# Performance work log

Measured on AMD Instinct MI355X. Metric: run time of the kernel, lower is better.

Reference implementation:

```python
import jax, jax.numpy as jnp
import numpy as np

LAYERS, BLOCKS = 10, 4
RC, DC, SC, EC, CLASSES = 32, 32, 256, 256, 256
KS = 2
OUTPUT_LENGTH = 4096


def _dilations():
    ds = []
    init = 1
    for _b in range(BLOCKS):
        nd = 1
        for _i in range(LAYERS):
            ds.append((nd, init))
            init = nd
            nd *= 2
    return ds

DILATIONS = _dilations()


def dilate(x, dilation, init_dilation):
    # Faithful port of pytorch-wavenet dilate(): folds time into batch (or back)
    # by the ratio dilation/init_dilation, front-padding with zeros if needed.
    n, c, l = x.shape
    if dilation == init_dilation:
        return x
    if dilation > init_dilation:
        r = dilation // init_dilation
        new_l = -(-l // r) * r  # ceil to multiple of r
        if new_l != l:
            x = jnp.pad(x, ((0, 0), (0, 0), (new_l - l, 0)))  # pad_start=True
            l = new_l
        l_new, n_new = l // r, n * r
    else:
        r = init_dilation // dilation
        l_new, n_new = l * r, n // r
    x = jnp.transpose(x, (1, 2, 0)).reshape(c, l_new, n_new)  # (c, l, n) view
    return jnp.transpose(x, (2, 0, 1))


def conv2tap(x, w):
    # valid Conv1d, kernel_size=2, no bias; x: [n,c,l], w: [o,c,2]
    return jax.lax.conv_general_dilated(x, w, (1,), 'VALID',
                                        dimension_numbers=('NCH', 'OIH', 'NCH'))


def conv1x1(x, w):
    # 1x1 Conv1d as einsum; x: [n,c,l], w: [o,c]
    return jnp.einsum('ncl,oc->nol', x, w)


def setup_inputs() -> dict:
    key = jax.random.key(0)
    ks = jax.random.split(key, 10)
    nl = LAYERS * BLOCKS
    s = 0.05
    return {
        'x_input': jax.random.normal(ks[0], (8, CLASSES, 16384), jnp.float32),
        'start_w': jax.random.normal(ks[1], (RC, CLASSES, 1), jnp.float32) * s,
        'filter_w': jax.random.normal(ks[2], (nl, DC, RC, KS), jnp.float32) * s,
        'gate_w': jax.random.normal(ks[3], (nl, DC, RC, KS), jnp.float32) * s,
        'residual_w': jax.random.normal(ks[4], (nl, RC, DC, 1), jnp.float32) * s,
        'skip_w': jax.random.normal(ks[5], (nl, SC, DC, 1), jnp.float32) * s,
        'end1_w': jax.random.normal(ks[6], (EC, SC, 1), jnp.float32) * s,
        'end1_b': jnp.zeros((EC,), jnp.float32),
        'end2_w': jax.random.normal(ks[7], (CLASSES, EC, 1), jnp.float32) * s,
        'end2_b': jnp.zeros((CLASSES,), jnp.float32),
    }


def reference(x_input, start_w, filter_w, gate_w, residual_w, skip_w,
              end1_w, end1_b, end2_w, end2_b):
    x = conv1x1(x_input, start_w[:, :, 0])
    x_skip = None
    for i, (d, d0) in enumerate(DILATIONS):
        xr = dilate(x, d, d0)
        f = jnp.tanh(conv2tap(xr, filter_w[i]))
        g = jax.nn.sigmoid(conv2tap(xr, gate_w[i]))
        x = f * g
        xs = dilate(x, 1, d) if x.shape[2] != 1 else x
        # NOTE: the source never reassigns `skip`, so its try/except always
        # falls to the except branch and only the LAST layer's skip survives.
        x_skip = conv1x1(xs, skip_w[i][:, :, 0])
        x = conv1x1(x, residual_w[i][:, :, 0]) + xr[:, :, KS - 1:]
    y = jax.nn.relu(x_skip)
    y = jax.nn.relu(conv1x1(y, end1_w[:, :, 0]) + end1_b[None, :, None])
    y = conv1x1(y, end2_w[:, :, 0]) + end2_b[None, :, None]
    n, c, _l = y.shape
    y = y[:, :, -OUTPUT_LENGTH:]
    return jnp.transpose(y, (0, 2, 1)).reshape(n * OUTPUT_LENGTH, c)
```

## Files before the change

### kernel.cpp

```cpp
#include <hip/hip_runtime.h>
#include <hip/hip_bf16.h>
#include <math.h>


#define TS   8192
#define T0   8188
#define NB   8
#define RCH  32
#define CLS  256
#define TOUT 4096

#define OFF_WBLOB 0
#define OFF_ST    204800
#define OFF_SK    212992
#define OFF_E1T   221184
#define OFF_E2T   286720
#define OFF_XA    352256
#define OFF_XB    (OFF_XA + NB*RCH*TS)
#define OFF_H1    (OFF_XB + NB*RCH*TS)
#define OFF_E1    (OFF_H1 + NB*256*TOUT)

__device__ __forceinline__ float tanh_fast(float x) {
    float e = __expf(2.0f * x);
    return 1.0f - 2.0f / (e + 1.0f);
}
__device__ __forceinline__ float sigmoid_fast(float x) {
    return 1.0f / (1.0f + __expf(-x));
}

__global__ void repack_kernel(const float* __restrict__ start_w,
                              const float* __restrict__ filter_w,
                              const float* __restrict__ gate_w,
                              const float* __restrict__ residual_w,
                              const float* __restrict__ skip_w,
                              const float* __restrict__ end1_w,
                              const float* __restrict__ end2_w,
                              float* __restrict__ ws) {
    int id = blockIdx.x * 256 + threadIdx.x;
    if (id < 204800) {
        int l = id / 5120, r = id % 5120;
        float v;
        if (r < 4096) {
            const float* src = (r < 2048) ? filter_w : gate_w;
            int rr = r & 2047;
            int ic = rr >> 6, k = (rr >> 5) & 1, oc = rr & 31;
            v = src[((l * 32 + oc) * 32 + ic) * 2 + k];
        } else {
            int rr = r - 4096;
            int ic = rr >> 5, oc = rr & 31;
            v = residual_w[(l * 32 + oc) * 32 + ic];
        }
        ws[OFF_WBLOB + id] = v;
    } else if (id < 204800 + 8192) {
        int r = id - 204800;
        int ic = r >> 5, oc = r & 31;
        ws[OFF_ST + r] = start_w[oc * 256 + ic];
    } else if (id < 212992 + 8192) {
        int r = id - 212992;
        int dc = r >> 8, sc = r & 255;
        ws[OFF_SK + r] = skip_w[(39 * 256 + sc) * 32 + dc];
    } else if (id < 221184 + 65536) {
        int r = id - 221184;
        int sc = r >> 8, ec = r & 255;
        ws[OFF_E1T + r] = end1_w[ec * 256 + sc];
    } else if (id < 286720 + 65536) {
        int r = id - 286720;
        int ec = r >> 8, cc = r & 255;
        ws[OFF_E2T + r] = end2_w[cc * 256 + ec];
    }
}

__global__ __launch_bounds__(256) void start_kernel(const float* __restrict__ xin,
                                                    const float* __restrict__ st,
                                                    float* __restrict__ xout) {
    int t = blockIdx.x * 256 + threadIdx.x;
    int og = blockIdx.y;
    int b = blockIdx.z;
    if (t >= T0) return;
    const float* xi = xin + (size_t)b * 256 * 16384 + (16384 - T0) + t;
    const float* wb = st + og * 16;
    float acc[16];
#pragma unroll
    for (int c = 0; c < 16; c++) acc[c] = 0.f;
#pragma unroll 4
    for (int ic = 0; ic < 256; ic++) {
        float xv = xi[ic * 16384];
        const float* w = wb + ic * 32;
#pragma unroll
        for (int c = 0; c < 16; c++) acc[c] = fmaf(w[c], xv, acc[c]);
    }
    float* xo = xout + ((size_t)(b * RCH) + og * 16) * TS + t;
#pragma unroll
    for (int c = 0; c < 16; c++) xo[c * TS] = acc[c];
}

__global__ __launch_bounds__(256) void layer_kernel(const float* __restrict__ xin,
                                                    float* __restrict__ xout,
                                                    const float* __restrict__ wl,
                                                    int d, int Tout) {
    __shared__ float hs[32][64];
    int tx = threadIdx.x;
    int cg = __builtin_amdgcn_readfirstlane(threadIdx.y);
    int t  = blockIdx.x * 64 + tx;
    int b  = blockIdx.y;
    bool act = (t < Tout);

    const float* xi = xin + (size_t)(b * RCH) * TS + t;
    const float* wf = wl +        cg * 8;
    const float* wg = wl + 2048 + cg * 8;
    const float* wr = wl + 4096 + cg * 8;

    float accf[8], accg[8];
#pragma unroll
    for (int j = 0; j < 8; j++) { accf[j] = 0.f; accg[j] = 0.f; }

#pragma unroll 4
    for (int ic = 0; ic < 32; ic++) {
        float a = xi[ic * TS];
        float c = xi[ic * TS + d];
        const float* w0 = wf + ic * 64;
        const float* w1 = wg + ic * 64;
#pragma unroll
        for (int j = 0; j < 8; j++) accf[j] = fmaf(w0[j],      a, accf[j]);
#pragma unroll
        for (int j = 0; j < 8; j++) accf[j] = fmaf(w0[32 + j], c, accf[j]);
#pragma unroll
        for (int j = 0; j < 8; j++) accg[j] = fmaf(w1[j],      a, accg[j]);
#pragma unroll
        for (int j = 0; j < 8; j++) accg[j] = fmaf(w1[32 + j], c, accg[j]);
    }

#pragma unroll
    for (int j = 0; j < 8; j++)
        hs[cg * 8 + j][tx] = tanh_fast(accf[j]) * sigmoid_fast(accg[j]);
    __syncthreads();

    float accr[8];
#pragma unroll
    for (int j = 0; j < 8; j++) accr[j] = xi[(cg * 8 + j) * TS + d];
#pragma unroll 4
    for (int ic = 0; ic < 32; ic++) {
        float h = hs[ic][tx];
        const float* w = wr + ic * 32;
#pragma unroll
        for (int j = 0; j < 8; j++) accr[j] = fmaf(w[j], h, accr[j]);
    }

    if (act) {
        float* xo = xout + ((size_t)(b * RCH) + cg * 8) * TS + t;
#pragma unroll
        for (int j = 0; j < 8; j++) xo[j * TS] = accr[j];
    }
}

__global__ __launch_bounds__(256) void layer_last_kernel(const float* __restrict__ xin,
                                                         float* __restrict__ xout,
                                                         const float* __restrict__ wl,
                                                         int d, int Tout) {
    int tx = threadIdx.x;
    int cg = __builtin_amdgcn_readfirstlane(threadIdx.y);
    int t  = blockIdx.x * 64 + tx;
    int b  = blockIdx.y;
    if (t >= Tout) return;
    const float* xi = xin + (size_t)(b * RCH) * TS + t;
    const float* wf = wl +        cg * 8;
    const float* wg = wl + 2048 + cg * 8;

    float accf[8], accg[8];
#pragma unroll
    for (int j = 0; j < 8; j++) { accf[j] = 0.f; accg[j] = 0.f; }
#pragma unroll 4
    for (int ic = 0; ic < 32; ic++) {
        float a = xi[ic * TS];
        float c = xi[ic * TS + d];
        const float* w0 = wf + ic * 64;
        const float* w1 = wg + ic * 64;
#pragma unroll
        for (int j = 0; j < 8; j++) accf[j] = fmaf(w0[j],      a, accf[j]);
#pragma unroll
        for (int j = 0; j < 8; j++) accf[j] = fmaf(w0[32 + j], c, accf[j]);
#pragma unroll
        for (int j = 0; j < 8; j++) accg[j] = fmaf(w1[j],      a, accg[j]);
#pragma unroll
        for (int j = 0; j < 8; j++) accg[j] = fmaf(w1[32 + j], c, accg[j]);
    }
    float* xo = xout + ((size_t)(b * RCH) + cg * 8) * TS + t;
#pragma unroll
    for (int j = 0; j < 8; j++)
        xo[j * TS] = tanh_fast(accf[j]) * sigmoid_fast(accg[j]);
}

__global__ __launch_bounds__(256) void skip_kernel(const float* __restrict__ xin,
                                                   const float* __restrict__ sk,
                                                   float* __restrict__ h1) {
    int t = blockIdx.x * 256 + threadIdx.x;
    int sg = blockIdx.y;
    int b = blockIdx.z;
    const float* xi = xin + (size_t)(b * RCH) * TS + t;
    const float* wb = sk + sg * 32;
    float acc[32];
#pragma unroll
    for (int j = 0; j < 32; j++) acc[j] = 0.f;
#pragma unroll 4
    for (int dc = 0; dc < 32; dc++) {
        float xv = xi[dc * TS];
        const float* w = wb + dc * 256;
#pragma unroll
        for (int j = 0; j < 32; j++) acc[j] = fmaf(w[j], xv, acc[j]);
    }
    float* ho = h1 + ((size_t)(b * 256) + sg * 32) * TOUT + t;
#pragma unroll
    for (int j = 0; j < 32; j++) ho[j * TOUT] = fmaxf(acc[j], 0.f);
}

__global__ __launch_bounds__(256) void end1_kernel(const float* __restrict__ h1,
                                                   const float* __restrict__ e1t,
                                                   const float* __restrict__ b1,
                                                   float* __restrict__ e1) {
    int t = blockIdx.x * 256 + threadIdx.x;
    int eg = blockIdx.y;
    int b = blockIdx.z;
    const float* hp = h1 + (size_t)(b * 256) * TOUT + t;
    const float* wb = e1t + eg * 32;
    float acc[32];
#pragma unroll
    for (int j = 0; j < 32; j++) acc[j] = b1[eg * 32 + j];
#pragma unroll 4
    for (int sc = 0; sc < 256; sc++) {
        float xv = hp[sc * TOUT];
        const float* w = wb + sc * 256;
#pragma unroll
        for (int j = 0; j < 32; j++) acc[j] = fmaf(w[j], xv, acc[j]);
    }
    float* ep = e1 + ((size_t)(b * 256) + eg * 32) * TOUT + t;
#pragma unroll
    for (int j = 0; j < 32; j++) ep[j * TOUT] = fmaxf(acc[j], 0.f);
}

__global__ __launch_bounds__(256) void end2_kernel(const float* __restrict__ e1,
                                                   const float* __restrict__ e2t,
                                                   const float* __restrict__ b2,
                                                   float* __restrict__ out) {
    int t = blockIdx.x * 256 + threadIdx.x;
    int cg = blockIdx.y;
    int b = blockIdx.z;
    const float* ep = e1 + (size_t)(b * 256) * TOUT + t;
    const float* wb = e2t + cg * 32;
    float acc[32];
#pragma unroll
    for (int j = 0; j < 32; j++) acc[j] = b2[cg * 32 + j];
#pragma unroll 4
    for (int ec = 0; ec < 256; ec++) {
        float xv = ep[ec * TOUT];
        const float* w = wb + ec * 256;
#pragma unroll
        for (int j = 0; j < 32; j++) acc[j] = fmaf(w[j], xv, acc[j]);
    }
    float* op = out + ((size_t)(b * TOUT + t)) * CLS + cg * 32;
#pragma unroll
    for (int j = 0; j < 8; j++)
        ((float4*)op)[j] = make_float4(acc[4*j], acc[4*j+1], acc[4*j+2], acc[4*j+3]);
}

extern "C" void kernel_launch(void* const* d_in, const int* in_sizes, int n_in,
                              void* d_out, int out_size, void* d_ws, size_t ws_size,
                              hipStream_t stream) {
    const float* x_input    = (const float*)d_in[0];
    const float* start_w    = (const float*)d_in[1];
    const float* filter_w   = (const float*)d_in[2];
    const float* gate_w     = (const float*)d_in[3];
    const float* residual_w = (const float*)d_in[4];
    const float* skip_w     = (const float*)d_in[5];
    const float* end1_w     = (const float*)d_in[6];
    const float* end1_b     = (const float*)d_in[7];
    const float* end2_w     = (const float*)d_in[8];
    const float* end2_b     = (const float*)d_in[9];
    float* ws  = (float*)d_ws;
    float* out = (float*)d_out;

    repack_kernel<<<dim3((352256 + 255) / 256), 256, 0, stream>>>(
        start_w, filter_w, gate_w, residual_w, skip_w, end1_w, end2_w, ws);

    start_kernel<<<dim3(32, 2, NB), 256, 0, stream>>>(
        x_input, ws + OFF_ST, ws + OFF_XA);

    float* bufs[2] = { ws + OFF_XA, ws + OFF_XB };
    int cur = 0;
    int Tin = T0;
    int cnt = 0;
    for (int bl = 0; bl < 4; bl++) {
        int dd = 1;
        for (int i = 0; i < 10; i++) {
            int Tout_l = Tin - dd;
            dim3 grid((Tout_l + 63) / 64, NB);
            dim3 blk(64, 4);
            if (cnt < 39) {
                layer_kernel<<<grid, blk, 0, stream>>>(
                    bufs[cur], bufs[cur ^ 1], ws + OFF_WBLOB + (size_t)cnt * 5120, dd, Tout_l);
            } else {
                layer_last_kernel<<<grid, blk, 0, stream>>>(
                    bufs[cur], bufs[cur ^ 1], ws + OFF_WBLOB + (size_t)cnt * 5120, dd, Tout_l);
            }
            cur ^= 1;
            Tin = Tout_l;
            dd *= 2;
            cnt++;
        }
    }

    skip_kernel<<<dim3(16, 8, NB), 256, 0, stream>>>(bufs[cur], ws + OFF_SK, ws + OFF_H1);
    end1_kernel<<<dim3(16, 8, NB), 256, 0, stream>>>(ws + OFF_H1, ws + OFF_E1T, end1_b, ws + OFF_E1);
    end2_kernel<<<dim3(16, 8, NB), 256, 0, stream>>>(ws + OFF_E1, ws + OFF_E2T, end2_b, out);
}
```

Baseline: 909.0 us.

## Fuse each dilation block into LDS-resident head and tail kernels

Replaces the 40 per-layer launches with 8 launches. Each block of ten layers is split in two. A head kernel runs dilations 1 to 16 on a haloed time tile held in shared memory and writes its output transposed into 32 phase-separated subsequences. A tail kernel then runs dilations 32 to 512 as dilations 1 to 16 over one subsequence, also in shared memory. The aim is to cut global memory traffic and launch overhead, at the cost of recomputing halos, extra register pressure from 32-wide per-thread outputs, and poor thread utilisation in the halo and tail phases.

```diff
diff --git a/kernel.cpp b/kernel.cpp
--- a/kernel.cpp
+++ b/kernel.cpp
@@ -1,5 +1,4 @@
 #include <hip/hip_runtime.h>
-#include <hip/hip_bf16.h>
 #include <math.h>
 
 
@@ -16,8 +15,8 @@
 #define OFF_E1T   221184
 #define OFF_E2T   286720
 #define OFF_XA    352256
-#define OFF_XB    (OFF_XA + NB*RCH*TS)
-#define OFF_H1    (OFF_XB + NB*RCH*TS)
+#define OFF_XSUB  (OFF_XA + NB*RCH*TS)
+#define OFF_H1    (OFF_XSUB + NB*RCH*TS)
 #define OFF_E1    (OFF_H1 + NB*256*TOUT)
 
 __device__ __forceinline__ float tanh_fast(float x) {
@@ -94,100 +93,158 @@
     for (int c = 0; c < 16; c++) xo[c * TS] = acc[c];
 }
 
-__global__ __launch_bounds__(256) void layer_kernel(const float* __restrict__ xin,
-                                                    float* __restrict__ xout,
-                                                    const float* __restrict__ wl,
-                                                    int d, int Tout) {
-    __shared__ float hs[32][64];
-    int tx = threadIdx.x;
-    int cg = __builtin_amdgcn_readfirstlane(threadIdx.y);
-    int t  = blockIdx.x * 64 + tx;
-    int b  = blockIdx.y;
-    bool act = (t < Tout);
-
-    const float* xi = xin + (size_t)(b * RCH) * TS + t;
-    const float* wf = wl +        cg * 8;
-    const float* wg = wl + 2048 + cg * 8;
-    const float* wr = wl + 4096 + cg * 8;
-
-    float accf[8], accg[8];
-#pragma unroll
-    for (int j = 0; j < 8; j++) { accf[j] = 0.f; accg[j] = 0.f; }
-
-#pragma unroll 4
-    for (int ic = 0; ic < 32; ic++) {
-        float a = xi[ic * TS];
-        float c = xi[ic * TS + d];
-        const float* w0 = wf + ic * 64;
-        const float* w1 = wg + ic * 64;
-#pragma unroll
-        for (int j = 0; j < 8; j++) accf[j] = fmaf(w0[j],      a, accf[j]);
-#pragma unroll
-        for (int j = 0; j < 8; j++) accf[j] = fmaf(w0[32 + j], c, accf[j]);
-#pragma unroll
-        for (int j = 0; j < 8; j++) accg[j] = fmaf(w1[j],      a, accg[j]);
-#pragma unroll
-        for (int j = 0; j < 8; j++) accg[j] = fmaf(w1[32 + j], c, accg[j]);
-    }
-
-#pragma unroll
-    for (int j = 0; j < 8; j++)
-        hs[cg * 8 + j][tx] = tanh_fast(accf[j]) * sigmoid_fast(accg[j]);
+template<int LDSW>
+__device__ __forceinline__ void layer_slot(const float* Xs, int p, int d,
+                                           const float* __restrict__ wf,
+                                           const float* __restrict__ wg,
+                                           const float* __restrict__ wr,
+                                           float out[32], bool h_only) {
+    float h[32];
+#pragma unroll
+    for (int grp = 0; grp < 4; ++grp) {
+        float f[8], g[8];
+#pragma unroll
+        for (int j = 0; j < 8; ++j) { f[j] = 0.f; g[j] = 0.f; }
+#pragma unroll 4
+        for (int ic = 0; ic < 32; ++ic) {
+            const float a = Xs[ic * LDSW + p];
+            const float c = Xs[ic * LDSW + p + d];
+            const float* w0 = wf + ic * 64 + grp * 8;
+            const float* w1 = wg + ic * 64 + grp * 8;
+#pragma unroll
+            for (int j = 0; j < 8; ++j) {
+                f[j] = fmaf(w0[j],      a, f[j]);
+                f[j] = fmaf(w0[32 + j], c, f[j]);
+                g[j] = fmaf(w1[j],      a, g[j]);
+                g[j] = fmaf(w1[32 + j], c, g[j]);
+            }
+        }
+#pragma unroll
+        for (int j = 0; j < 8; ++j)
+            h[grp * 8 + j] = tanh_fast(f[j]) * sigmoid_fast(g[j]);
+    }
+    if (h_only) {
+#pragma unroll
+        for (int oc = 0; oc < 32; ++oc) out[oc] = h[oc];
+        return;
+    }
+#pragma unroll
+    for (int grp = 0; grp < 4; ++grp) {
+        float r[8];
+#pragma unroll
+        for (int j = 0; j < 8; ++j)
+            r[j] = Xs[(grp * 8 + j) * LDSW + p + d];
+        const float* w2 = wr + grp * 8;
+#pragma unroll 4
+        for (int ic = 0; ic < 32; ++ic) {
+            const float hv = h[ic];
+#pragma unroll
+            for (int j = 0; j < 8; ++j)
+                r[j] = fmaf(w2[ic * 32 + j], hv, r[j]);
+        }
+#pragma unroll
+        for (int j = 0; j < 8; ++j) out[grp * 8 + j] = r[j];
+    }
+}
+
+__global__ __launch_bounds__(256) void head_kernel(const float* __restrict__ X,
+                                                   float* __restrict__ Xsub,
+                                                   const float* __restrict__ wl0,
+                                                   int Tin) {
+    __shared__ float Xs[32 * 288];
+    const int tid = threadIdx.x;
+    const int b   = blockIdx.y;
+    const int c0  = blockIdx.x * 256;
+    const int Lw  = min(288, Tin - c0);
+
+    const float* xb = X + (size_t)b * (RCH * TS) + c0;
+    for (int idx = tid; idx < 32 * 288; idx += 256) {
+        int ch = idx / 288, p = idx - ch * 288;
+        if (p < Lw) Xs[ch * 288 + p] = xb[(size_t)ch * TS + p];
+    }
     __syncthreads();
 
-    float accr[8];
-#pragma unroll
-    for (int j = 0; j < 8; j++) accr[j] = xi[(cg * 8 + j) * TS + d];
-#pragma unroll 4
-    for (int ic = 0; ic < 32; ic++) {
-        float h = hs[ic][tx];
-        const float* w = wr + ic * 32;
-#pragma unroll
-        for (int j = 0; j < 8; j++) accr[j] = fmaf(w[j], h, accr[j]);
-    }
-
-    if (act) {
-        float* xo = xout + ((size_t)(b * RCH) + cg * 8) * TS + t;
-#pragma unroll
-        for (int j = 0; j < 8; j++) xo[j * TS] = accr[j];
-    }
-}
-
-__global__ __launch_bounds__(256) void layer_last_kernel(const float* __restrict__ xin,
-                                                         float* __restrict__ xout,
-                                                         const float* __restrict__ wl,
-                                                         int d, int Tout) {
-    int tx = threadIdx.x;
-    int cg = __builtin_amdgcn_readfirstlane(threadIdx.y);
-    int t  = blockIdx.x * 64 + tx;
-    int b  = blockIdx.y;
-    if (t >= Tout) return;
-    const float* xi = xin + (size_t)(b * RCH) * TS + t;
-    const float* wf = wl +        cg * 8;
-    const float* wg = wl + 2048 + cg * 8;
-
-    float accf[8], accg[8];
-#pragma unroll
-    for (int j = 0; j < 8; j++) { accf[j] = 0.f; accg[j] = 0.f; }
-#pragma unroll 4
-    for (int ic = 0; ic < 32; ic++) {
-        float a = xi[ic * TS];
-        float c = xi[ic * TS + d];
-        const float* w0 = wf + ic * 64;
-        const float* w1 = wg + ic * 64;
-#pragma unroll
-        for (int j = 0; j < 8; j++) accf[j] = fmaf(w0[j],      a, accf[j]);
-#pragma unroll
-        for (int j = 0; j < 8; j++) accf[j] = fmaf(w0[32 + j], c, accf[j]);
-#pragma unroll
-        for (int j = 0; j < 8; j++) accg[j] = fmaf(w1[j],      a, accg[j]);
-#pragma unroll
-        for (int j = 0; j < 8; j++) accg[j] = fmaf(w1[32 + j], c, accg[j]);
-    }
-    float* xo = xout + ((size_t)(b * RCH) + cg * 8) * TS + t;
-#pragma unroll
-    for (int j = 0; j < 8; j++)
-        xo[j * TS] = tanh_fast(accf[j]) * sigmoid_fast(accg[j]);
+    int w = Lw;
+    for (int s = 0; s < 5; ++s) {
+        const int d  = 1 << s;
+        const int nw = w - d;
+        const float* wf = wl0 + s * 5120;
+
+        float out0[32];
+        const bool a0 = (tid < nw);
+        if (a0) layer_slot<288>(Xs, tid, d, wf, wf + 2048, wf + 4096, out0, false);
+
+        float out1[32];
+        const int  p1 = 256 + (tid >> 3);
+        const bool a1 = (nw > 256) && ((tid & 7) == 0) && (p1 < nw);
+        if (nw > 256) {
+            if (a1) layer_slot<288>(Xs, p1, d, wf, wf + 2048, wf + 4096, out1, false);
+        }
+        __syncthreads();
+        if (a0) {
+#pragma unroll
+            for (int oc = 0; oc < 32; ++oc) Xs[oc * 288 + tid] = out0[oc];
+        }
+        if (a1) {
+#pragma unroll
+            for (int oc = 0; oc < 32; ++oc) Xs[oc * 288 + p1] = out1[oc];
+        }
+        __syncthreads();
+        w = nw;
+    }
+
+    const int ow = min(256, w);
+    if (tid < ow) {
+        const int t = c0 + tid, rr = t & 31, ii = t >> 5;
+        float* xs = Xsub + ((size_t)(b * 32) * 32 + rr) * 256 + ii;
+#pragma unroll
+        for (int oc = 0; oc < 32; ++oc)
+            xs[(size_t)oc * (32 * 256)] = Xs[oc * 288 + tid];
+    }
+}
+
+__global__ __launch_bounds__(256) void tail_kernel(const float* __restrict__ Xsub,
+                                                   float* __restrict__ X,
+                                                   const float* __restrict__ wl5,
+                                                   int Tin, int last) {
+    __shared__ float Xs[32 * 256];
+    const int tid = threadIdx.x;
+    const int r   = blockIdx.x;
+    const int b   = blockIdx.y;
+    const int L   = (Tin - r + 31) >> 5;
+
+    const float* xs = Xsub + ((size_t)(b * 32) * 32 + r) * 256;
+    for (int idx = tid; idx < 32 * 256; idx += 256) {
+        int ch = idx >> 8, i = idx & 255;
+        if (i < L) Xs[ch * 256 + i] = xs[(size_t)ch * (32 * 256) + i];
+    }
+    __syncthreads();
+
+    int w = L;
+    for (int s = 0; s < 5; ++s) {
+        const int dd = 1 << s;
+        const int nw = w - dd;
+        const float* wf = wl5 + s * 5120;
+        const bool ho = (last != 0) && (s == 4);
+
+        float out0[32];
+        const bool a0 = (tid < nw);
+        if (a0) layer_slot<256>(Xs, tid, dd, wf, wf + 2048, wf + 4096, out0, ho);
+        __syncthreads();
+        if (a0) {
+#pragma unroll
+            for (int oc = 0; oc < 32; ++oc) Xs[oc * 256 + tid] = out0[oc];
+        }
+        __syncthreads();
+        w = nw;
+    }
+
+    if (tid < w) {
+        const int t = (tid << 5) + r;
+        float* xp = X + (size_t)b * (RCH * TS) + t;
+#pragma unroll
+        for (int oc = 0; oc < 32; ++oc) xp[(size_t)oc * TS] = Xs[oc * 256 + tid];
+    }
 }
 
 __global__ __launch_bounds__(256) void skip_kernel(const float* __restrict__ xin,
@@ -284,31 +341,18 @@
     start_kernel<<<dim3(32, 2, NB), 256, 0, stream>>>(
         x_input, ws + OFF_ST, ws + OFF_XA);
 
-    float* bufs[2] = { ws + OFF_XA, ws + OFF_XB };
-    int cur = 0;
+    float* xa   = ws + OFF_XA;
+    float* xsub = ws + OFF_XSUB;
     int Tin = T0;
-    int cnt = 0;
-    for (int bl = 0; bl < 4; bl++) {
-        int dd = 1;
-        for (int i = 0; i < 10; i++) {
-            int Tout_l = Tin - dd;
-            dim3 grid((Tout_l + 63) / 64, NB);
-            dim3 blk(64, 4);
-            if (cnt < 39) {
-                layer_kernel<<<grid, blk, 0, stream>>>(
-                    bufs[cur], bufs[cur ^ 1], ws + OFF_WBLOB + (size_t)cnt * 5120, dd, Tout_l);
-            } else {
-                layer_last_kernel<<<grid, blk, 0, stream>>>(
-                    bufs[cur], bufs[cur ^ 1], ws + OFF_WBLOB + (size_t)cnt * 5120, dd, Tout_l);
-            }
-            cur ^= 1;
-            Tin = Tout_l;
-            dd *= 2;
-            cnt++;
-        }
-    }
-
-    skip_kernel<<<dim3(16, 8, NB), 256, 0, stream>>>(bufs[cur], ws + OFF_SK, ws + OFF_H1);
+    for (int sb = 0; sb < 4; ++sb) {
+        const float* wb = ws + OFF_WBLOB + (size_t)sb * 51200;
+        int Th = Tin - 31;
+        head_kernel<<<dim3((Th + 255) / 256, NB), 256, 0, stream>>>(xa, xsub, wb, Tin);
+        tail_kernel<<<dim3(32, NB), 256, 0, stream>>>(xsub, xa, wb + 25600, Th, (sb == 3) ? 1 : 0);
+        Tin = Th - 992;
+    }
+
+    skip_kernel<<<dim3(16, 8, NB), 256, 0, stream>>>(xa, ws + OFF_SK, ws + OFF_H1);
     end1_kernel<<<dim3(16, 8, NB), 256, 0, stream>>>(ws + OFF_H1, ws + OFF_E1T, end1_b, ws + OFF_E1);
     end2_kernel<<<dim3(16, 8, NB), 256, 0, stream>>>(ws + OFF_E1, ws + OFF_E2T, end2_b, out);
 }
```

Result: slower. 2.073 ms (+128.1%).
